# Performance work log

Measured on AMD Instinct MI355X. Metric: run time of the kernel, lower is better.

Reference implementation:

```python
import jax, jax.numpy as jnp
import numpy as np
from jax import lax

B, T = 256, 256
FD = (768, 74, 35)      # text, audio, vision input feature dims
HD = (128, 64, 64)      # LSTM hidden sizes
LEN = sum(HD)           # 256, fused feature dim
TW = 2                  # time_window
EXT = TW * LEN + 1      # 513, extended_dim
RANK = 24
OUT = 1


def setup_inputs() -> dict:
    key = jax.random.key(0)
    ks = iter(jax.random.split(key, 32))
    def n(shape, scale=0.05):
        return jax.random.normal(next(ks), shape, dtype=jnp.float32) * scale
    inp = {
        "text": n((B, T, FD[0]), 1.0),
        "audio": n((B, T, FD[1]), 1.0),
        "vision": n((B, T, FD[2]), 1.0),
    }
    # LSTM params per subnet: W_ih [4H, D], W_hh [4H, H], combined bias [4H]
    for tag, d, h in (("t", FD[0], HD[0]), ("a", FD[1], HD[1]), ("v", FD[2], HD[2])):
        inp[f"Wih_{tag}"] = n((4 * h, d))
        inp[f"Whh_{tag}"] = n((4 * h, h))
        inp[f"b_{tag}"] = n((4 * h,))
    inp["W1"] = n((RANK * OUT, LEN))
    inp["b1"] = n((RANK * OUT,))
    inp["W2"] = n((RANK * OUT, EXT))
    inp["b2"] = n((RANK * OUT,))
    inp["fw"] = n((1, RANK), 1.0)  # fusion_weights, xavier_normal-like
    return inp


def _lstm_seq(x, Wih, Whh, b):
    # x: [B, T, D] -> all hidden states [B, T, H]; torch gate order i,f,g,o
    Bn = x.shape[0]
    H = Whh.shape[1]
    h0 = jnp.zeros((Bn, H), x.dtype)
    def step(carry, xt):
        h, c = carry
        g = xt @ Wih.T + h @ Whh.T + b
        i, f, gg, o = jnp.split(g, 4, axis=-1)
        c = jax.nn.sigmoid(f) * c + jax.nn.sigmoid(i) * jnp.tanh(gg)
        h = jax.nn.sigmoid(o) * jnp.tanh(c)
        return (h, c), h
    _, hs = lax.scan(step, (h0, h0), jnp.swapaxes(x, 0, 1))
    return jnp.swapaxes(hs, 0, 1)


def reference(text, audio, vision,
              Wih_t, Whh_t, b_t, Wih_a, Whh_a, b_a, Wih_v, Whh_v, b_v,
              W1, b1, W2, b2, fw):
    # SubNets (dropout is identity in eval mode)
    audio_h = _lstm_seq(audio, Wih_a, Whh_a, b_a)
    video_h = _lstm_seq(vision, Wih_v, Whh_v, b_v)
    text_h = _lstm_seq(text, Wih_t, Whh_t, b_t)
    z = jnp.concatenate((audio_h, video_h, text_h), axis=2)  # [B, T, LEN]
    # time_extend with time_window=2: [ones, z[:, i], z[:, (i+1) % T]]
    ones = jnp.ones((z.shape[0], z.shape[1], 1), z.dtype)
    shifts = [jnp.roll(z, -j, axis=1) for j in range(TW)]
    z_ext = jnp.concatenate([ones] + shifts, axis=2)  # [B, T, EXT]
    # fusion loop over idx (stride=1 -> all T), vectorized as batched GEMM + mean
    a = jnp.einsum('btl,rl->btr', z, W1) + b1          # [B, T, RANK*OUT]
    bb = jnp.einsum('bte,re->btr', z_ext, W2) + b2     # [B, T, RANK*OUT]
    z_fusion = (a * bb).mean(axis=1)                   # sum_i/len(idx)
    z_fusion = z_fusion.reshape(-1, RANK, OUT)
    z_output = jnp.einsum('r,bro->bo', fw[0], z_fusion)
    output = z_output.reshape(-1, OUT)
    norm = jnp.sum(jnp.linalg.norm(z.reshape(z.shape[0], -1), axis=1)) / z.shape[0]
    return output, norm
```

## Files before the change

kernel.cpp:

```cpp
#include <hip/hip_runtime.h>
#include <math.h>


typedef unsigned short ushortT;
typedef short bf16x8 __attribute__((ext_vector_type(8)));
typedef float f32x4 __attribute__((ext_vector_type(4)));

__device__ __forceinline__ unsigned int f2bf(float f) {
  unsigned int u = __float_as_uint(f);
  u += 0x7FFFu + ((u >> 16) & 1u);
  return u >> 16;
}
__device__ __forceinline__ unsigned int pk2bf(float lo, float hi) {
  return f2bf(lo) | (f2bf(hi) << 16);
}
__device__ __forceinline__ float bf2f(ushortT u) {
  return __uint_as_float(((unsigned int)u) << 16);
}

template <int KP, int KIN>
__global__ __launch_bounds__(256) void pad_cvt_k(const float* __restrict__ src,
                                                 ushortT* __restrict__ dst, int total) {
  const int i = blockIdx.x * 256 + threadIdx.x;
  if (i >= total) return;
  if constexpr (KP == KIN) {
    dst[i] = (ushortT)f2bf(src[i]);
  } else {
    const int row = i / KP, c = i - row * KP;
    dst[i] = (c < KIN) ? (ushortT)f2bf(src[(size_t)row * KIN + c]) : (ushortT)0;
  }
}

#define SA2 40
__global__ __launch_bounds__(512) void gemm_text2_k(const float* __restrict__ X,
                                                    const ushortT* __restrict__ W16,
                                                    const float* __restrict__ bias,
                                                    ushortT* __restrict__ Y16) {
  const int K = 768;
  __shared__ __align__(16) ushortT As[128 * SA2];
  __shared__ __align__(16) ushortT Bs[256 * SA2];
  const unsigned int lin = blockIdx.x;
  const int gb = (int)(lin >> 4), rb = (int)(lin & 15);
  const int m0 = (gb * 8 + (rb & 7)) * 128;
  const int n0 = (rb >> 3) * 256;
  const int tid = threadIdx.x;
  const int wave = tid >> 6, lane = tid & 63;
  const int wr = wave >> 2, wc = wave & 3;
  const int lm = lane & 15, lq = lane >> 4;
  const int arow = tid >> 2, aq = (tid & 3) * 8;
  const int brow = tid >> 1, bq = (tid & 1) * 16;

  const float*   Xp = X + (size_t)(m0 + arow) * K + aq;
  const ushortT* Wp = W16 + (size_t)(n0 + brow) * K + bq;
  uint4* As_w = (uint4*)&As[arow * SA2 + aq];
  uint4* Bs_w = (uint4*)&Bs[brow * SA2 + bq];

  f32x4 acc[4][4];
#pragma unroll
  for (int i = 0; i < 4; i++)
#pragma unroll
    for (int j = 0; j < 4; j++) acc[i][j] = (f32x4){0.f, 0.f, 0.f, 0.f};

  for (int k0 = 0; k0 < K; k0 += 32) {
    const float4 a0 = *(const float4*)(Xp + k0);
    const float4 a1 = *(const float4*)(Xp + k0 + 4);
    const uint4 b0v = *(const uint4*)(Wp + k0);
    const uint4 b1v = *(const uint4*)(Wp + k0 + 8);
    __syncthreads();
    uint4 ao;
    ao.x = pk2bf(a0.x, a0.y); ao.y = pk2bf(a0.z, a0.w);
    ao.z = pk2bf(a1.x, a1.y); ao.w = pk2bf(a1.z, a1.w);
    As_w[0] = ao;
    Bs_w[0] = b0v;
    Bs_w[1] = b1v;
    __syncthreads();
    bf16x8 af[4], bfv[4];
#pragma unroll
    for (int mt = 0; mt < 4; mt++)
      af[mt] = *(const bf16x8*)&As[(wr * 64 + mt * 16 + lm) * SA2 + lq * 8];
#pragma unroll
    for (int nt = 0; nt < 4; nt++)
      bfv[nt] = *(const bf16x8*)&Bs[(wc * 64 + nt * 16 + lm) * SA2 + lq * 8];
#pragma unroll
    for (int mt = 0; mt < 4; mt++)
#pragma unroll
      for (int nt = 0; nt < 4; nt++)
        acc[mt][nt] = __builtin_amdgcn_mfma_f32_16x16x32_bf16(af[mt], bfv[nt], acc[mt][nt], 0, 0, 0);
  }
  float biasv[4];
#pragma unroll
  for (int nt = 0; nt < 4; nt++) biasv[nt] = bias[n0 + wc * 64 + nt * 16 + lm];
  const int bb = m0 >> 8;
  const int mq16 = ((bb & 15) >> 2) * 16;
  const int mr2 = bb & 3;
  const size_t chunk0 = (size_t)((bb >> 4) * 256) * 8192;
  const int tbase = (m0 & 255) + wr * 64 + lq * 4;
#pragma unroll
  for (int nt = 0; nt < 4; nt++) {
    const int C = n0 + wc * 64 + nt * 16 + lm;
    const int g = C >> 7, cc = C & 127;
    const int off_nt = (g >> 1) * 4096 + ((cc >> 4) * 64 + mq16 + (cc & 15)) * 8 +
                       (g & 1) * 4 + mr2;
#pragma unroll
    for (int mt = 0; mt < 4; mt++) {
      const size_t a0 = chunk0 + (size_t)(tbase + mt * 16) * 8192 + off_nt;
#pragma unroll
      for (int r = 0; r < 4; r++)
        Y16[a0 + (size_t)r * 8192] = (ushortT)f2bf(acc[mt][nt][r] + biasv[nt]);
    }
  }
}

template <int KP>
__global__ __launch_bounds__(256) void gemm_xp_k(const ushortT* __restrict__ A16,
                                                 const ushortT* __restrict__ B16,
                                                 const float* __restrict__ bias,
                                                 ushortT* __restrict__ Y16) {
  constexpr int SB = KP + 8;
  __shared__ __align__(16) ushortT As[128 * SB];
  __shared__ __align__(16) ushortT Bs[128 * SB];
  const int n0 = blockIdx.x * 128;
  const int m0 = blockIdx.y * 128;
  const int tid = threadIdx.x;
  const int srow = tid >> 1, shalf = tid & 1;
  const int wave = tid >> 6, lane = tid & 63;
  const int wr = wave >> 1, wc = wave & 1;
  const int lm = lane & 15, lq = lane >> 4;

  const uint4* ap = (const uint4*)(A16 + (size_t)(m0 + srow) * KP + shalf * (KP / 2));
  const uint4* bp = (const uint4*)(B16 + (size_t)(n0 + srow) * KP + shalf * (KP / 2));
  uint4* aw = (uint4*)&As[srow * SB + shalf * (KP / 2)];
  uint4* bw = (uint4*)&Bs[srow * SB + shalf * (KP / 2)];
#pragma unroll
  for (int i = 0; i < KP / 16; i++) { aw[i] = ap[i]; bw[i] = bp[i]; }
  __syncthreads();

  constexpr int KC = KP / 32;
  f32x4 acc[4][4];
#pragma unroll
  for (int i = 0; i < 4; i++)
#pragma unroll
    for (int j = 0; j < 4; j++) acc[i][j] = (f32x4){0.f, 0.f, 0.f, 0.f};
#pragma unroll
  for (int ks = 0; ks < KC; ks++) {
    bf16x8 af[4], bfv[4];
#pragma unroll
    for (int mt = 0; mt < 4; mt++)
      af[mt] = *(const bf16x8*)&As[(wr * 64 + mt * 16 + lm) * SB + ks * 32 + lq * 8];
#pragma unroll
    for (int nt = 0; nt < 4; nt++)
      bfv[nt] = *(const bf16x8*)&Bs[(wc * 64 + nt * 16 + lm) * SB + ks * 32 + lq * 8];
#pragma unroll
    for (int mt = 0; mt < 4; mt++)
#pragma unroll
      for (int nt = 0; nt < 4; nt++)
        acc[mt][nt] = __builtin_amdgcn_mfma_f32_16x16x32_bf16(af[mt], bfv[nt], acc[mt][nt], 0, 0, 0);
  }
  float biasv[4];
#pragma unroll
  for (int nt = 0; nt < 4; nt++) biasv[nt] = bias[n0 + wc * 64 + nt * 16 + lm];
  const int bb = m0 >> 8;
  const int mq16 = ((bb & 15) >> 2) * 16;
  const int mr2 = bb & 3;
  const size_t chunk0 = (size_t)((bb >> 4) * 256) * 4096;
  const int tbase = (m0 & 255) + wr * 64 + lq * 4;
#pragma unroll
  for (int nt = 0; nt < 4; nt++) {
    const int C = n0 + wc * 64 + nt * 16 + lm;
    const int g = C >> 6, cc = C & 63;
    const int off_nt = (g >> 1) * 2048 + ((cc >> 4) * 64 + mq16 + (cc & 15)) * 8 +
                       (g & 1) * 4 + mr2;
#pragma unroll
    for (int mt = 0; mt < 4; mt++) {
      const size_t a0 = chunk0 + (size_t)(tbase + mt * 16) * 4096 + off_nt;
#pragma unroll
      for (int r = 0; r < 4; r++)
        Y16[a0 + (size_t)r * 4096] = (ushortT)f2bf(acc[mt][nt][r] + biasv[nt]);
    }
  }
}

__device__ __forceinline__ void bar_lgkm() {
  asm volatile("s_waitcnt lgkmcnt(0)" ::: "memory");
  __builtin_amdgcn_sched_barrier(0);
  __builtin_amdgcn_s_barrier();
  __builtin_amdgcn_sched_barrier(0);
}

template <int H, int COFF, int CW>
__device__ __forceinline__ void recur_impl4(const ushortT* __restrict__ xp,
                                            const ushortT* __restrict__ Whh,
                                            ushortT* __restrict__ z,
                                            int bblk, char* smem_) {
  constexpr int KC = H / 32;
  constexpr int HP = H + 8;
  constexpr int RING = 6;
  constexpr int CRB = H / 8;
  constexpr int FPT = (64 * CRB) / 512;
  constexpr int TS = CW * 64 * 16;
  ushortT* hbuf = (ushortT*)smem_;
  const int tid = threadIdx.x;
  const int s = tid >> 6, lane = tid & 63;
  const int lm = lane & 15, lq = lane >> 4;
  const int b0 = bblk * 16;
  const bool comp = (s < CW);
  const ushortT* xg = xp + (size_t)(bblk * 256) * TS + tid * 8;

  bf16x8 bw[4][KC];
  if (comp) {
#pragma unroll
    for (int g = 0; g < 4; g++)
#pragma unroll
      for (int kc = 0; kc < KC; kc++) {
        const int n = g * H + s * 16 + lm;
        bw[g][kc] = *(const bf16x8*)(Whh + (size_t)n * H + kc * 32 + lq * 8);
      }
  }
  for (int i = tid; i < 16 * HP; i += 512) hbuf[(RING - 1) * 16 * HP + i] = 0;

  uint4 gA[2], gB[2];
  if (comp) {
    gA[0] = *(const uint4*)(xg);
    gA[1] = *(const uint4*)(xg + TS / 2);
    gB[0] = *(const uint4*)(xg + TS);
    gB[1] = *(const uint4*)(xg + TS + TS / 2);
  }
  float cst[4] = {0.f, 0.f, 0.f, 0.f};
  __syncthreads();

  auto step = [&](int t, uint4 (&gCur)[2]) {
    if (t >= 4 && (t & 3) == 0) {
      const int t0 = t - 4;
#pragma unroll
      for (int i = 0; i < FPT; i++) {
        const int q = i * 512 + tid;
        const int m = q / (4 * CRB), j = (q / CRB) & 3, cr = q % CRB;
        const uint4 v = *(const uint4*)&hbuf[((t0 + j) % RING) * 16 * HP + m * HP + cr * 8];
        *(uint4*)&z[((size_t)(b0 + m) * 256 + t0 + j) * 256 + COFF + cr * 8] = v;
      }
    }
    if (comp) {
      unsigned int w[8] = {gCur[0].x, gCur[0].y, gCur[0].z, gCur[0].w,
                           gCur[1].x, gCur[1].y, gCur[1].z, gCur[1].w};
      float ad[4][4];
#pragma unroll
      for (int g = 0; g < 4; g++)
#pragma unroll
        for (int r = 0; r < 4; r++) {
          const unsigned int ww = w[g * 2 + (r >> 1)];
          ad[g][r] = __uint_as_float((r & 1) ? (ww & 0xffff0000u) : (ww << 16));
        }
      const int tn = (t + 2 < 256) ? t + 2 : 255;
      gCur[0] = *(const uint4*)(xg + (size_t)tn * TS);
      gCur[1] = *(const uint4*)(xg + (size_t)tn * TS + TS / 2);
      const ushortT* hb = &hbuf[((t + RING - 1) % RING) * 16 * HP + lm * HP];
      bf16x8 af[KC];
#pragma unroll
      for (int kc = 0; kc < KC; kc++) af[kc] = *(const bf16x8*)(hb + kc * 32 + lq * 8);
      f32x4 acc[4];
#pragma unroll
      for (int g = 0; g < 4; g++) acc[g] = (f32x4){0.f, 0.f, 0.f, 0.f};
#pragma unroll
      for (int kc = 0; kc < KC; kc++)
#pragma unroll
        for (int g = 0; g < 4; g++)
          acc[g] = __builtin_amdgcn_mfma_f32_16x16x32_bf16(af[kc], bw[g][kc], acc[g], 0, 0, 0);
      ushortT* hw = &hbuf[(t % RING) * 16 * HP];
      const int col = s * 16 + lm;
#pragma unroll
      for (int r = 0; r < 4; r++) {
        const float iv = acc[0][r] + ad[0][r];
        const float fv = acc[1][r] + ad[1][r];
        const float gg = acc[2][r] + ad[2][r];
        const float ov = acc[3][r] + ad[3][r];
        const float ei = __expf(-iv), ef = __expf(-fv), eg = __expf(-2.f * gg);
        const float pi = 1.f + ei, pf = 1.f + ef, pg = 1.f + eg;
        const float cc = (cst[r] * pi * pg + (1.f - eg) * pf) *
                         __builtin_amdgcn_rcpf(pf * pi * pg);
        cst[r] = cc;
        const float ec = __expf(-2.f * cc), eo = __expf(-ov);
        const float hv = (1.f - ec) * __builtin_amdgcn_rcpf((1.f + eo) * (1.f + ec));
        hw[(lq * 4 + r) * HP + col] = (ushortT)f2bf(hv);
      }
    }
    bar_lgkm();
  };

  for (int t = 0; t < 256; t += 2) {
    step(t, gA);
    step(t + 1, gB);
  }
  {
    const int t0 = 252;
#pragma unroll
    for (int i = 0; i < FPT; i++) {
      const int q = i * 512 + tid;
      const int m = q / (4 * CRB), j = (q / CRB) & 3, cr = q % CRB;
      const uint4 v = *(const uint4*)&hbuf[((t0 + j) % RING) * 16 * HP + m * HP + cr * 8];
      *(uint4*)&z[((size_t)(b0 + m) * 256 + t0 + j) * 256 + COFF + cr * 8] = v;
    }
  }
}

__global__ __launch_bounds__(512, 1) void recur4_k(const ushortT* __restrict__ xpt,
                                                   const ushortT* __restrict__ xpa,
                                                   const ushortT* __restrict__ xpv_,
                                                   const ushortT* __restrict__ Wt,
                                                   const ushortT* __restrict__ Wa,
                                                   const ushortT* __restrict__ Wv,
                                                   ushortT* __restrict__ z) {
  extern __shared__ char smem[];
  const int bid = blockIdx.x;
  if (bid < 16) recur_impl4<128, 128, 8>(xpt, Wt, z, bid, smem);
  else if (bid < 32) recur_impl4<64, 0, 4>(xpa, Wa, z, bid - 16, smem);
  else recur_impl4<64, 64, 4>(xpv_, Wv, z, bid - 32, smem);
}

__global__ __launch_bounds__(192) void fusion_k(const ushortT* __restrict__ z,
                                                const float* __restrict__ W1,
                                                const float* __restrict__ b1,
                                                const float* __restrict__ W2,
                                                const float* __restrict__ b2,
                                                const float* __restrict__ fw,
                                                float* __restrict__ s_acc,
                                                float* __restrict__ sumsq) {
  __shared__ __align__(16) float zs[256 * 36];
  __shared__ float red[8];
  const int tid = threadIdx.x;
  const int b = blockIdx.x >> 3;
  const int t0 = (blockIdx.x & 7) * 32;
  const ushortT* zb = z + (size_t)b * 65536;
  float sq = 0.0f;
  for (int idx = tid; idx < 33 * 256; idx += 192) {
    const int row = idx >> 8, k = idx & 255;
    int t = t0 + row; if (t >= 256) t -= 256;
    const float v = bf2f(zb[t * 256 + k]);
    zs[k * 36 + row] = v;
    if (row < 32) sq += v * v;
  }
  __syncthreads();
  const int dg = tid >> 3;
  const int rg = tid & 7;
  const float* w1p = W1 + dg * 256;
  const float* w2p = W2 + dg * 513;
  float aa[4] = {}, ab1[4] = {}, ab2[4] = {};
#pragma unroll 4
  for (int k = 0; k < 256; k++) {
    const float w1v = w1p[k];
    const float w21 = w2p[1 + k];
    const float w22 = w2p[257 + k];
    const float* zr = &zs[k * 36 + (rg << 2)];
    const float4 za = *(const float4*)zr;
    const float z4 = zr[4];
    aa[0]  += za.x * w1v; aa[1]  += za.y * w1v; aa[2]  += za.z * w1v; aa[3]  += za.w * w1v;
    ab1[0] += za.x * w21; ab1[1] += za.y * w21; ab1[2] += za.z * w21; ab1[3] += za.w * w21;
    ab2[0] += za.y * w22; ab2[1] += za.z * w22; ab2[2] += za.w * w22; ab2[3] += z4   * w22;
  }
  const float b1v = b1[dg];
  const float b2v = b2[dg] + w2p[0];
  const float fwv = fw[dg];
  float s = 0.0f;
#pragma unroll
  for (int i = 0; i < 4; i++) {
    const float a  = aa[i] + b1v;
    const float bb = ab1[i] + ab2[i] + b2v;
    s += a * bb;
  }
  s *= fwv;
#pragma unroll
  for (int off = 32; off > 0; off >>= 1) {
    s  += __shfl_down(s, off);
    sq += __shfl_down(sq, off);
  }
  const int wid = tid >> 6;
  if ((tid & 63) == 0) { red[wid * 2] = s; red[wid * 2 + 1] = sq; }
  __syncthreads();
  if (tid == 0) {
    atomicAdd(&s_acc[b], red[0] + red[2] + red[4]);
    atomicAdd(&sumsq[b], red[1] + red[3] + red[5]);
  }
}

__global__ __launch_bounds__(256) void final_k(const float* __restrict__ s_acc,
                                               const float* __restrict__ sumsq,
                                               float* __restrict__ out) {
  __shared__ float red[4];
  const int tid = threadIdx.x;
  out[tid] = s_acc[tid] * (1.0f / 256.0f);
  float sq = sqrtf(sumsq[tid]);
#pragma unroll
  for (int off = 32; off > 0; off >>= 1) sq += __shfl_down(sq, off);
  if ((tid & 63) == 0) red[tid >> 6] = sq;
  __syncthreads();
  if (tid == 0) out[256] = (red[0] + red[1] + red[2] + red[3]) * (1.0f / 256.0f);
}

extern "C" void kernel_launch(void* const* d_in, const int* in_sizes, int n_in,
                              void* d_out, int out_size, void* d_ws, size_t ws_size,
                              hipStream_t stream) {
  const float* text   = (const float*)d_in[0];
  const float* audio  = (const float*)d_in[1];
  const float* vision = (const float*)d_in[2];
  const float* Wih_t  = (const float*)d_in[3];
  const float* Whh_t  = (const float*)d_in[4];
  const float* b_t    = (const float*)d_in[5];
  const float* Wih_a  = (const float*)d_in[6];
  const float* Whh_a  = (const float*)d_in[7];
  const float* b_a    = (const float*)d_in[8];
  const float* Wih_v  = (const float*)d_in[9];
  const float* Whh_v  = (const float*)d_in[10];
  const float* b_v    = (const float*)d_in[11];
  const float* W1     = (const float*)d_in[12];
  const float* b1     = (const float*)d_in[13];
  const float* W2     = (const float*)d_in[14];
  const float* b2     = (const float*)d_in[15];
  const float* fw     = (const float*)d_in[16];

  ushortT* xpt = (ushortT*)d_ws;
  ushortT* xpa = xpt + (size_t)33554432;
  ushortT* xpv = xpa + (size_t)16777216;
  ushortT* z16 = xpv + (size_t)16777216;
  float* s_acc = (float*)(z16 + (size_t)16777216);
  float* sumsq = s_acc + 256;
  ushortT* WhhT16 = (ushortT*)(sumsq + 256);
  ushortT* WhhA16 = WhhT16 + 65536;
  ushortT* WhhV16 = WhhA16 + 16384;
  ushortT* A16a  = z16;
  ushortT* A16v  = A16a + (size_t)6291456;
  ushortT* Wt768 = A16v + (size_t)4194304;
  ushortT* WA16  = Wt768 + 393216;
  ushortT* WV16  = WA16 + 24576;

  hipMemsetAsync(s_acc, 0, 512 * sizeof(float), stream);

  pad_cvt_k<768, 768><<<1536, 256, 0, stream>>>(Wih_t, Wt768, 512 * 768);
  pad_cvt_k<128, 128><<<256, 256, 0, stream>>>(Whh_t, WhhT16, 512 * 128);
  pad_cvt_k<64, 64><<<64, 256, 0, stream>>>(Whh_a, WhhA16, 256 * 64);
  pad_cvt_k<64, 64><<<64, 256, 0, stream>>>(Whh_v, WhhV16, 256 * 64);
  pad_cvt_k<96, 74><<<96, 256, 0, stream>>>(Wih_a, WA16, 256 * 96);
  pad_cvt_k<64, 35><<<64, 256, 0, stream>>>(Wih_v, WV16, 256 * 64);
  pad_cvt_k<96, 74><<<24576, 256, 0, stream>>>(audio, A16a, 65536 * 96);
  pad_cvt_k<64, 35><<<16384, 256, 0, stream>>>(vision, A16v, 65536 * 64);

  gemm_text2_k<<<1024, 512, 0, stream>>>(text, Wt768, b_t, xpt);
  gemm_xp_k<96><<<dim3(2, 512), 256, 0, stream>>>(A16a, WA16, b_a, xpa);
  gemm_xp_k<64><<<dim3(2, 512), 256, 0, stream>>>(A16v, WV16, b_v, xpv);
  recur4_k<<<48, 512, 26112, stream>>>(xpt, xpa, xpv, WhhT16, WhhA16, WhhV16, z16);
  fusion_k<<<2048, 192, 0, stream>>>(z16, W1, b1, W2, b2, fw, s_acc, sumsq);
  final_k<<<1, 256, 0, stream>>>(s_acc, sumsq, (float*)d_out);
}
```

Measured before the change: 846.5 us.

## Interleave gate rows in input weights and fuse prep conversions into one kernel

The input-projection weights are converted with rows permuted so the four gates of each hidden unit sit next to each other. The projection GEMMs can then write plain row-major outputs instead of a scattered tiled layout, and the recurrence reads four gate values per hidden unit as one 8-byte load per batch row. All the separate bf16 conversion kernels are merged into one launch to cut launch overhead. The trade-off is that the recurrence now makes narrower, more strided global loads, while the GEMM epilogue writes become coalesced.

```diff
diff --git a/kernel.cpp b/kernel.cpp
--- a/kernel.cpp
+++ b/kernel.cpp
@@ -18,17 +18,39 @@
   return __uint_as_float(((unsigned int)u) << 16);
 }
 
-template <int KP, int KIN>
-__global__ __launch_bounds__(256) void pad_cvt_k(const float* __restrict__ src,
-                                                 ushortT* __restrict__ dst, int total) {
-  const int i = blockIdx.x * 256 + threadIdx.x;
+template <int KP, int KIN, int HR>
+__device__ __forceinline__ void cvt_range(const float* __restrict__ src,
+                                          ushortT* __restrict__ dst,
+                                          int i, int total) {
   if (i >= total) return;
-  if constexpr (KP == KIN) {
+  if constexpr (HR == 0 && KP == KIN) {
     dst[i] = (ushortT)f2bf(src[i]);
   } else {
     const int row = i / KP, c = i - row * KP;
-    dst[i] = (c < KIN) ? (ushortT)f2bf(src[(size_t)row * KIN + c]) : (ushortT)0;
-  }
+    const int srow = HR ? ((row & 3) * HR + (row >> 2)) : row;
+    const float v = (c < KIN) ? src[(size_t)srow * KIN + c] : 0.f;
+    dst[i] = (ushortT)f2bf(v);
+  }
+}
+
+__global__ __launch_bounds__(256) void prep_k(
+    const float* __restrict__ Wih_t, const float* __restrict__ Whh_t,
+    const float* __restrict__ Wih_a, const float* __restrict__ Whh_a,
+    const float* __restrict__ Wih_v, const float* __restrict__ Whh_v,
+    const float* __restrict__ audio, const float* __restrict__ vision,
+    ushortT* __restrict__ Wt768, ushortT* __restrict__ WhhT16,
+    ushortT* __restrict__ WA16, ushortT* __restrict__ WhhA16,
+    ushortT* __restrict__ WV16, ushortT* __restrict__ WhhV16,
+    ushortT* __restrict__ A16a, ushortT* __restrict__ A16v) {
+  const int b = blockIdx.x, tid = threadIdx.x;
+  if (b < 1536)       cvt_range<768, 768, 128>(Wih_t, Wt768, b * 256 + tid, 393216);
+  else if (b < 1792)  cvt_range<128, 128, 0>(Whh_t, WhhT16, (b - 1536) * 256 + tid, 65536);
+  else if (b < 1856)  cvt_range<64, 64, 0>(Whh_a, WhhA16, (b - 1792) * 256 + tid, 16384);
+  else if (b < 1920)  cvt_range<64, 64, 0>(Whh_v, WhhV16, (b - 1856) * 256 + tid, 16384);
+  else if (b < 2016)  cvt_range<96, 74, 64>(Wih_a, WA16, (b - 1920) * 256 + tid, 24576);
+  else if (b < 2080)  cvt_range<64, 35, 64>(Wih_v, WV16, (b - 2016) * 256 + tid, 16384);
+  else if (b < 26656) cvt_range<96, 74, 0>(audio, A16a, (b - 2080) * 256 + tid, 6291456);
+  else                cvt_range<64, 35, 0>(vision, A16v, (b - 26656) * 256 + tid, 4194304);
 }
 
 #define SA2 40
@@ -36,7 +58,7 @@
                                                     const ushortT* __restrict__ W16,
                                                     const float* __restrict__ bias,
                                                     ushortT* __restrict__ Y16) {
-  const int K = 768;
+  const int K = 768, N = 512;
   __shared__ __align__(16) ushortT As[128 * SA2];
   __shared__ __align__(16) ushortT Bs[256 * SA2];
   const unsigned int lin = blockIdx.x;
@@ -89,29 +111,24 @@
   }
   float biasv[4];
 #pragma unroll
-  for (int nt = 0; nt < 4; nt++) biasv[nt] = bias[n0 + wc * 64 + nt * 16 + lm];
-  const int bb = m0 >> 8;
-  const int mq16 = ((bb & 15) >> 2) * 16;
-  const int mr2 = bb & 3;
-  const size_t chunk0 = (size_t)((bb >> 4) * 256) * 8192;
-  const int tbase = (m0 & 255) + wr * 64 + lq * 4;
-#pragma unroll
   for (int nt = 0; nt < 4; nt++) {
     const int C = n0 + wc * 64 + nt * 16 + lm;
-    const int g = C >> 7, cc = C & 127;
-    const int off_nt = (g >> 1) * 4096 + ((cc >> 4) * 64 + mq16 + (cc & 15)) * 8 +
-                       (g & 1) * 4 + mr2;
-#pragma unroll
-    for (int mt = 0; mt < 4; mt++) {
-      const size_t a0 = chunk0 + (size_t)(tbase + mt * 16) * 8192 + off_nt;
+    biasv[nt] = bias[((C & 3) << 7) + (C >> 2)];
+  }
+#pragma unroll
+  for (int mt = 0; mt < 4; mt++) {
+#pragma unroll
+    for (int nt = 0; nt < 4; nt++) {
+      const int row0 = m0 + wr * 64 + mt * 16 + lq * 4;
+      const int col = n0 + wc * 64 + nt * 16 + lm;
 #pragma unroll
       for (int r = 0; r < 4; r++)
-        Y16[a0 + (size_t)r * 8192] = (ushortT)f2bf(acc[mt][nt][r] + biasv[nt]);
-    }
-  }
-}
-
-template <int KP>
+        Y16[(size_t)(row0 + r) * N + col] = (ushortT)f2bf(acc[mt][nt][r] + biasv[nt]);
+    }
+  }
+}
+
+template <int KP, int LOG2H>
 __global__ __launch_bounds__(256) void gemm_xp_k(const ushortT* __restrict__ A16,
                                                  const ushortT* __restrict__ B16,
                                                  const float* __restrict__ bias,
@@ -158,24 +175,19 @@
   }
   float biasv[4];
 #pragma unroll
-  for (int nt = 0; nt < 4; nt++) biasv[nt] = bias[n0 + wc * 64 + nt * 16 + lm];
-  const int bb = m0 >> 8;
-  const int mq16 = ((bb & 15) >> 2) * 16;
-  const int mr2 = bb & 3;
-  const size_t chunk0 = (size_t)((bb >> 4) * 256) * 4096;
-  const int tbase = (m0 & 255) + wr * 64 + lq * 4;
-#pragma unroll
   for (int nt = 0; nt < 4; nt++) {
     const int C = n0 + wc * 64 + nt * 16 + lm;
-    const int g = C >> 6, cc = C & 63;
-    const int off_nt = (g >> 1) * 2048 + ((cc >> 4) * 64 + mq16 + (cc & 15)) * 8 +
-                       (g & 1) * 4 + mr2;
-#pragma unroll
-    for (int mt = 0; mt < 4; mt++) {
-      const size_t a0 = chunk0 + (size_t)(tbase + mt * 16) * 4096 + off_nt;
+    biasv[nt] = bias[((C & 3) << LOG2H) + (C >> 2)];
+  }
+#pragma unroll
+  for (int mt = 0; mt < 4; mt++) {
+#pragma unroll
+    for (int nt = 0; nt < 4; nt++) {
+      const int row0 = m0 + wr * 64 + mt * 16 + lq * 4;
+      const int col = n0 + wc * 64 + nt * 16 + lm;
 #pragma unroll
       for (int r = 0; r < 4; r++)
-        Y16[a0 + (size_t)r * 4096] = (ushortT)f2bf(acc[mt][nt][r] + biasv[nt]);
+        Y16[(size_t)(row0 + r) * 256 + col] = (ushortT)f2bf(acc[mt][nt][r] + biasv[nt]);
     }
   }
 }
@@ -188,23 +200,24 @@
 }
 
 template <int H, int COFF, int CW>
-__device__ __forceinline__ void recur_impl4(const ushortT* __restrict__ xp,
+__device__ __forceinline__ void recur_impl5(const ushortT* __restrict__ xp,
                                             const ushortT* __restrict__ Whh,
                                             ushortT* __restrict__ z,
                                             int bblk, char* smem_) {
   constexpr int KC = H / 32;
+  constexpr int C4H = 4 * H;
   constexpr int HP = H + 8;
   constexpr int RING = 6;
   constexpr int CRB = H / 8;
   constexpr int FPT = (64 * CRB) / 512;
-  constexpr int TS = CW * 64 * 16;
+  constexpr int RS = 256 * C4H;
   ushortT* hbuf = (ushortT*)smem_;
   const int tid = threadIdx.x;
   const int s = tid >> 6, lane = tid & 63;
   const int lm = lane & 15, lq = lane >> 4;
   const int b0 = bblk * 16;
   const bool comp = (s < CW);
-  const ushortT* xg = xp + (size_t)(bblk * 256) * TS + tid * 8;
+  const ushortT* xb = xp + (size_t)(b0 + lq * 4) * RS + (s * 16 + lm) * 4;
 
   bf16x8 bw[4][KC];
   if (comp) {
@@ -218,17 +231,18 @@
   }
   for (int i = tid; i < 16 * HP; i += 512) hbuf[(RING - 1) * 16 * HP + i] = 0;
 
-  uint4 gA[2], gB[2];
+  uint2 gA[4], gB[4];
   if (comp) {
-    gA[0] = *(const uint4*)(xg);
-    gA[1] = *(const uint4*)(xg + TS / 2);
-    gB[0] = *(const uint4*)(xg + TS);
-    gB[1] = *(const uint4*)(xg + TS + TS / 2);
+#pragma unroll
+    for (int r = 0; r < 4; r++) {
+      gA[r] = *(const uint2*)(xb + (size_t)r * RS);
+      gB[r] = *(const uint2*)(xb + (size_t)r * RS + C4H);
+    }
   }
   float cst[4] = {0.f, 0.f, 0.f, 0.f};
   __syncthreads();
 
-  auto step = [&](int t, uint4 (&gCur)[2]) {
+  auto step = [&](int t, uint2 (&gCur)[4]) {
     if (t >= 4 && (t & 3) == 0) {
       const int t0 = t - 4;
 #pragma unroll
@@ -240,19 +254,19 @@
       }
     }
     if (comp) {
-      unsigned int w[8] = {gCur[0].x, gCur[0].y, gCur[0].z, gCur[0].w,
-                           gCur[1].x, gCur[1].y, gCur[1].z, gCur[1].w};
       float ad[4][4];
 #pragma unroll
-      for (int g = 0; g < 4; g++)
-#pragma unroll
-        for (int r = 0; r < 4; r++) {
-          const unsigned int ww = w[g * 2 + (r >> 1)];
-          ad[g][r] = __uint_as_float((r & 1) ? (ww & 0xffff0000u) : (ww << 16));
-        }
+      for (int r = 0; r < 4; r++) {
+        const unsigned int w0 = gCur[r].x, w1 = gCur[r].y;
+        ad[0][r] = __uint_as_float(w0 << 16);
+        ad[1][r] = __uint_as_float(w0 & 0xffff0000u);
+        ad[2][r] = __uint_as_float(w1 << 16);
+        ad[3][r] = __uint_as_float(w1 & 0xffff0000u);
+      }
       const int tn = (t + 2 < 256) ? t + 2 : 255;
-      gCur[0] = *(const uint4*)(xg + (size_t)tn * TS);
-      gCur[1] = *(const uint4*)(xg + (size_t)tn * TS + TS / 2);
+#pragma unroll
+      for (int r = 0; r < 4; r++)
+        gCur[r] = *(const uint2*)(xb + (size_t)r * RS + (size_t)tn * C4H);
       const ushortT* hb = &hbuf[((t + RING - 1) % RING) * 16 * HP + lm * HP];
       bf16x8 af[KC];
 #pragma unroll
@@ -302,7 +316,7 @@
   }
 }
 
-__global__ __launch_bounds__(512, 1) void recur4_k(const ushortT* __restrict__ xpt,
+__global__ __launch_bounds__(512, 1) void recur5_k(const ushortT* __restrict__ xpt,
                                                    const ushortT* __restrict__ xpa,
                                                    const ushortT* __restrict__ xpv_,
                                                    const ushortT* __restrict__ Wt,
@@ -311,9 +325,9 @@
                                                    ushortT* __restrict__ z) {
   extern __shared__ char smem[];
   const int bid = blockIdx.x;
-  if (bid < 16) recur_impl4<128, 128, 8>(xpt, Wt, z, bid, smem);
-  else if (bid < 32) recur_impl4<64, 0, 4>(xpa, Wa, z, bid - 16, smem);
-  else recur_impl4<64, 64, 4>(xpv_, Wv, z, bid - 32, smem);
+  if (bid < 16) recur_impl5<128, 128, 8>(xpt, Wt, z, bid, smem);
+  else if (bid < 32) recur_impl5<64, 0, 4>(xpa, Wa, z, bid - 16, smem);
+  else recur_impl5<64, 64, 4>(xpv_, Wv, z, bid - 32, smem);
 }
 
 __global__ __launch_bounds__(192) void fusion_k(const ushortT* __restrict__ z,
@@ -433,19 +447,15 @@
 
   hipMemsetAsync(s_acc, 0, 512 * sizeof(float), stream);
 
-  pad_cvt_k<768, 768><<<1536, 256, 0, stream>>>(Wih_t, Wt768, 512 * 768);
-  pad_cvt_k<128, 128><<<256, 256, 0, stream>>>(Whh_t, WhhT16, 512 * 128);
-  pad_cvt_k<64, 64><<<64, 256, 0, stream>>>(Whh_a, WhhA16, 256 * 64);
-  pad_cvt_k<64, 64><<<64, 256, 0, stream>>>(Whh_v, WhhV16, 256 * 64);
-  pad_cvt_k<96, 74><<<96, 256, 0, stream>>>(Wih_a, WA16, 256 * 96);
-  pad_cvt_k<64, 35><<<64, 256, 0, stream>>>(Wih_v, WV16, 256 * 64);
-  pad_cvt_k<96, 74><<<24576, 256, 0, stream>>>(audio, A16a, 65536 * 96);
-  pad_cvt_k<64, 35><<<16384, 256, 0, stream>>>(vision, A16v, 65536 * 64);
+  prep_k<<<43040, 256, 0, stream>>>(Wih_t, Whh_t, Wih_a, Whh_a, Wih_v, Whh_v,
+                                    audio, vision,
+                                    Wt768, WhhT16, WA16, WhhA16, WV16, WhhV16,
+                                    A16a, A16v);
 
   gemm_text2_k<<<1024, 512, 0, stream>>>(text, Wt768, b_t, xpt);
-  gemm_xp_k<96><<<dim3(2, 512), 256, 0, stream>>>(A16a, WA16, b_a, xpa);
-  gemm_xp_k<64><<<dim3(2, 512), 256, 0, stream>>>(A16v, WV16, b_v, xpv);
-  recur4_k<<<48, 512, 26112, stream>>>(xpt, xpa, xpv, WhhT16, WhhA16, WhhV16, z16);
+  gemm_xp_k<96, 6><<<dim3(2, 512), 256, 0, stream>>>(A16a, WA16, b_a, xpa);
+  gemm_xp_k<64, 6><<<dim3(2, 512), 256, 0, stream>>>(A16v, WV16, b_v, xpv);
+  recur5_k<<<48, 512, 26112, stream>>>(xpt, xpa, xpv, WhhT16, WhhA16, WhhV16, z16);
   fusion_k<<<2048, 192, 0, stream>>>(z16, W1, b1, W2, b2, fw, s_acc, sumsq);
   final_k<<<1, 256, 0, stream>>>(s_acc, sumsq, (float*)d_out);
 }
```

New measurement: 765.1 us. 9.6% less time.
